# Kernel optimization log

Hardware: AMD Instinct MI355X
Metric: run time of the kernel (lower is better)

The kernel has to match this reference:

```python
import jax, jax.numpy as jnp
import numpy as np

EPS = 1e-5

def setup_inputs() -> dict:
    key = jax.random.key(0)
    ks = jax.random.split(key, 5)
    B, C_clip, Hc, Wc = 8, 768, 24, 24
    C_rs, Hr, Wr = 256, 64, 64
    clip_feat = jax.random.normal(ks[0], (B, C_clip, Hc, Wc), dtype=jnp.float32)
    rs_feat = jax.random.normal(ks[1], (B, C_rs, Hr, Wr), dtype=jnp.float32)
    ln_gamma = jnp.ones((C_clip,), dtype=jnp.float32)
    ln_beta = jnp.zeros((C_clip,), dtype=jnp.float32)
    W = jax.random.normal(ks[2], (C_rs, C_clip), dtype=jnp.float32) * (1.0 / np.sqrt(C_clip))
    b = jax.random.normal(ks[3], (C_rs,), dtype=jnp.float32) * 0.01
    alpha = jnp.array([0.5], dtype=jnp.float32)
    return {"clip_feat": clip_feat, "rs_feat": rs_feat, "ln_gamma": ln_gamma,
            "ln_beta": ln_beta, "W": W, "b": b, "alpha": alpha}

def reference(clip_feat, rs_feat, ln_gamma, ln_beta, W, b, alpha):
    B, C_clip, Hc, Wc = clip_feat.shape
    _, C_rs, Hr, Wr = rs_feat.shape
    # tokens: [B, N_clip, C_clip]
    clip_flat = clip_feat.reshape(B, C_clip, Hc * Wc).transpose(0, 2, 1)
    mu = jnp.mean(clip_flat, axis=-1, keepdims=True)
    var = jnp.var(clip_flat, axis=-1, keepdims=True)
    clip_norm = (clip_flat - mu) * jax.lax.rsqrt(var + EPS) * ln_gamma + ln_beta
    # projection to rs_dim: [B, N_clip, C_rs]
    clip_proj = jnp.einsum('bnc,dc->bnd', clip_norm, W) + b
    # rs tokens: [B, N_rs, C_rs]
    rs_flat = rs_feat.reshape(B, C_rs, Hr * Wr).transpose(0, 2, 1)
    # attn_map: [B, N_clip, N_rs], softmax over N_clip (axis=1)
    attn = jnp.einsum('bnd,bmd->bnm', clip_proj, rs_flat)
    attn = jax.nn.softmax(attn, axis=1)
    # attended: [B, N_rs, C_rs]
    attended = jnp.einsum('bnm,bnd->bmd', attn, clip_proj)
    attended = attended.transpose(0, 2, 1).reshape(B, C_rs, Hr, Wr)
    return rs_feat + alpha * attended
```

## Files before the change

kernel.cpp:

```cpp
#include <hip/hip_runtime.h>
#include <hip/hip_bf16.h>

#define EPSF 1e-5f
#define SM_OFF 60.0f

typedef short short8 __attribute__((ext_vector_type(8)));
typedef float f32x4 __attribute__((ext_vector_type(4)));

__device__ __forceinline__ short f2bf(float x) {
    __hip_bfloat16 h = __float2bfloat16(x);
    return reinterpret_cast<short&>(h);
}
__device__ __forceinline__ float bf2f(short s) {
    __hip_bfloat16 h = reinterpret_cast<__hip_bfloat16&>(s);
    return __bfloat162float(h);
}
__device__ __forceinline__ unsigned int pk2(float lo, float hi) {
    return (unsigned int)(unsigned short)f2bf(lo)
         | ((unsigned int)(unsigned short)f2bf(hi) << 16);
}
__device__ __forceinline__ void gload_lds16(const short* g, short* lds) {
    __builtin_amdgcn_global_load_lds(
        (const __attribute__((address_space(1))) unsigned int*)g,
        (__attribute__((address_space(3))) unsigned int*)lds,
        16, 0, 0);
}

__global__ __launch_bounds__(256) void w_pack_kernel(
    const float* __restrict__ W,
    short* __restrict__ Wp_hi,
    short* __restrict__ Wp_lo)
{
    int t = blockIdx.x * 256 + threadIdx.x;
    int l15 = t & 15;
    int g   = (t >> 4) & 3;
    int kt  = (t >> 6) % 24;
    int nt  = t / 1536;
    const float* src = W + (size_t)(16 * nt + l15) * 768 + 32 * kt + 8 * g;
    short8 h8, l8;
    #pragma unroll
    for (int j = 0; j < 8; ++j) {
        float w = src[j];
        short h = f2bf(w);
        h8[j] = h;
        l8[j] = f2bf(w - bf2f(h));
    }
    *reinterpret_cast<short8*>(Wp_hi + (size_t)t * 8) = h8;
    *reinterpret_cast<short8*>(Wp_lo + (size_t)t * 8) = l8;
}

__global__ __launch_bounds__(512) void ln_proj_kernel(
    const float* __restrict__ clip,
    const float* __restrict__ gamma,
    const float* __restrict__ beta,
    const short* __restrict__ Wp_hi,
    const short* __restrict__ Wp_lo,
    const float* __restrict__ bias,
    short* __restrict__ proj,
    short* __restrict__ projT)
{
    __shared__ short xh[16][776];
    __shared__ short xl[16][776];
    __shared__ float redA[8][16];
    __shared__ float redB[8][16];
    __shared__ float muS[16], rsS[16];

    const int tid = threadIdx.x;
    const int bb = blockIdx.x >> 1;
    const int dh = blockIdx.x & 1;
    const int b  = bb / 36;
    const int n0 = (bb % 36) * 16;
    const int nl = tid & 15;
    const int cg = tid >> 4;
    const int w  = tid >> 6;
    const int l  = tid & 63;
    const int l15 = l & 15;
    const int g  = l >> 4;

    const float* base = clip + (size_t)b * 768 * 576 + n0 + nl;

    float x[24];
    float s1 = 0.f, s2 = 0.f;
    #pragma unroll
    for (int i = 0; i < 24; ++i) {
        x[i] = base[(size_t)(cg + 32 * i) * 576];
        s1 += x[i]; s2 += x[i] * x[i];
    }
    s1 += __shfl_xor(s1, 16); s2 += __shfl_xor(s2, 16);
    s1 += __shfl_xor(s1, 32); s2 += __shfl_xor(s2, 32);
    if (g == 0) { redA[w][l15] = s1; redB[w][l15] = s2; }
    __syncthreads();
    if (tid < 16) {
        float a = 0.f, q = 0.f;
        #pragma unroll
        for (int k = 0; k < 8; ++k) { a += redA[k][tid]; q += redB[k][tid]; }
        float mu = a * (1.f / 768.f);
        float var = q * (1.f / 768.f) - mu * mu;
        muS[tid] = mu; rsS[tid] = rsqrtf(var + EPSF);
    }
    __syncthreads();
    {
        float mu = muS[nl], rsg = rsS[nl];
        #pragma unroll
        for (int i = 0; i < 24; ++i) {
            int c = cg + 32 * i;
            float y = (x[i] - mu) * rsg * gamma[c] + beta[c];
            short hh = f2bf(y);
            xh[nl][c] = hh;
            xl[nl][c] = f2bf(y - bf2f(hh));
        }
    }
    __syncthreads();

    const int nt = 8 * dh + w;
    f32x4 acc = f32x4{0.f, 0.f, 0.f, 0.f};
    for (int kt = 0; kt < 24; ++kt) {
        short8 ah = *reinterpret_cast<const short8*>(&xh[l15][32 * kt + 8 * g]);
        short8 al = *reinterpret_cast<const short8*>(&xl[l15][32 * kt + 8 * g]);
        size_t off = ((size_t)((nt * 24 + kt) * 64 + l)) * 8;
        short8 bh = *reinterpret_cast<const short8*>(Wp_hi + off);
        short8 bl = *reinterpret_cast<const short8*>(Wp_lo + off);
        acc = __builtin_amdgcn_mfma_f32_16x16x32_bf16(ah, bh, acc, 0, 0, 0);
        acc = __builtin_amdgcn_mfma_f32_16x16x32_bf16(al, bh, acc, 0, 0, 0);
        acc = __builtin_amdgcn_mfma_f32_16x16x32_bf16(ah, bl, acc, 0, 0, 0);
    }

    {
        int d = 16 * nt + l15;
        float bb2 = bias[d];
        #pragma unroll
        for (int r = 0; r < 4; ++r) {
            int tok = n0 + 4 * g + r;
            short v = f2bf(acc[r] + bb2);
            proj[((size_t)b * 576 + tok) * 256 + d] = v;
            projT[((size_t)b * 256 + d) * 576 + tok] = v;
        }
    }
}

__global__ __launch_bounds__(256, 2) void attn_kernel(
    const short* __restrict__ proj,
    const short* __restrict__ projT,
    const float* __restrict__ rs,
    const float* __restrict__ alpha_p,
    float* __restrict__ out)
{
    __shared__ short Ks[2][32][256];
    __shared__ short VT[2][256][32];
    __shared__ unsigned int Pb[2][2][2][16][20];
    __shared__ float Rb[2][2][2][16];

    const int tid = threadIdx.x;
    const int b  = blockIdx.x >> 6;
    const int q0 = (blockIdx.x & 63) << 6;
    const int w   = tid >> 6;
    const int l   = tid & 63;
    const int l15 = l & 15;
    const int g   = l >> 4;
    const int qh  = w >> 1;
    const int kh  = w & 1;
    const int qb  = q0 + 32 * qh;

    const short* kbase  = proj  + (size_t)b * 576 * 256;
    const short* ktbase = projT + (size_t)b * 256 * 576;
    const float* rbase  = rs + (size_t)b * 256 * 4096;
    float* obase = out + (size_t)b * 256 * 4096;

    short8 qf[2][8];
    #pragma unroll
    for (int qt = 0; qt < 2; ++qt) {
        int qg = qb + 16 * qt + l15;
        #pragma unroll
        for (int dc = 0; dc < 8; ++dc) {
            short8 v;
            #pragma unroll
            for (int j = 0; j < 8; ++j)
                v[j] = f2bf(rbase[(size_t)(32 * dc + 8 * g + j) * 4096 + qg]);
            qf[qt][dc] = v;
        }
    }

    f32x4 acc[2][8];
    #pragma unroll
    for (int qt = 0; qt < 2; ++qt)
        #pragma unroll
        for (int dt = 0; dt < 8; ++dt) acc[qt][dt] = f32x4{0.f, 0.f, 0.f, 0.f};
    float rsum[2] = {0.f, 0.f};

    auto STAGE = [&](int c, int buf) {
        #pragma unroll
        for (int i = 0; i < 4; ++i) {
            int rr = 8 * w + 2 * i + (l >> 5);
            const short* src = kbase + ((size_t)(32 * c + rr) << 8)
                             + ((((l & 31) ^ (rr & 7))) << 3);
            gload_lds16(src, &Ks[buf][8 * w + 2 * i][0]);
        }
        #pragma unroll
        for (int i = 0; i < 4; ++i) {
            int d = 64 * w + 16 * i + (l >> 2);
            const short* src = ktbase + (size_t)d * 576 + 32 * c + 8 * (l & 3);
            gload_lds16(src, &VT[buf][64 * w + 16 * i][0]);
        }
    };

    STAGE(0, 0);
    __syncthreads();

    for (int c = 0; c < 18; ++c) {
        const int cur = c & 1;

        f32x4 s0{0.f,0.f,0.f,0.f}, s1{0.f,0.f,0.f,0.f};
        __builtin_amdgcn_s_setprio(1);
        #pragma unroll
        for (int dc = 0; dc < 8; ++dc) {
            int sw = (((4 * dc + g) ^ (l15 & 7))) * 8;
            short8 kf = *reinterpret_cast<const short8*>(&Ks[cur][16 * kh + l15][sw]);
            s0 = __builtin_amdgcn_mfma_f32_16x16x32_bf16(kf, qf[0][dc], s0, 0, 0, 0);
            s1 = __builtin_amdgcn_mfma_f32_16x16x32_bf16(kf, qf[1][dc], s1, 0, 0, 0);
        }
        __builtin_amdgcn_s_setprio(0);

        float p0[4], p1[4];
        #pragma unroll
        for (int r = 0; r < 4; ++r) {
            p0[r] = __expf(s0[r] - SM_OFF);
            p1[r] = __expf(s1[r] - SM_OFF);
            rsum[0] += p0[r]; rsum[1] += p1[r];
        }
        *reinterpret_cast<uint2*>(&Pb[cur][qh][0][l15][8 * kh + 2 * g]) =
            uint2{pk2(p0[0], p0[1]), pk2(p0[2], p0[3])};
        *reinterpret_cast<uint2*>(&Pb[cur][qh][1][l15][8 * kh + 2 * g]) =
            uint2{pk2(p1[0], p1[1]), pk2(p1[2], p1[3])};

        __syncthreads();

        if (c < 17) STAGE(c + 1, cur ^ 1);

        short8 pf0 = *reinterpret_cast<const short8*>(&Pb[cur][qh][0][l15][4 * g]);
        short8 pf1 = *reinterpret_cast<const short8*>(&Pb[cur][qh][1][l15][4 * g]);
        __builtin_amdgcn_s_setprio(1);
        #pragma unroll
        for (int dt = 0; dt < 8; ++dt) {
            short8 vf = *reinterpret_cast<const short8*>(
                &VT[cur][128 * kh + 16 * dt + l15][8 * g]);
            acc[0][dt] = __builtin_amdgcn_mfma_f32_16x16x32_bf16(vf, pf0, acc[0][dt], 0, 0, 0);
            acc[1][dt] = __builtin_amdgcn_mfma_f32_16x16x32_bf16(vf, pf1, acc[1][dt], 0, 0, 0);
        }
        __builtin_amdgcn_s_setprio(0);

        if (c < 17) __syncthreads();
    }

    #pragma unroll
    for (int qt = 0; qt < 2; ++qt) {
        rsum[qt] += __shfl_xor(rsum[qt], 16);
        rsum[qt] += __shfl_xor(rsum[qt], 32);
    }
    if (g == 0) {
        Rb[qh][kh][0][l15] = rsum[0];
        Rb[qh][kh][1][l15] = rsum[1];
    }
    __syncthreads();
    float av = alpha_p[0];
    float inv0 = av / (Rb[qh][0][0][l15] + Rb[qh][1][0][l15]);
    float inv1 = av / (Rb[qh][0][1][l15] + Rb[qh][1][1][l15]);

    #pragma unroll
    for (int qt = 0; qt < 2; ++qt) {
        float inv = qt ? inv1 : inv0;
        int qg = qb + 16 * qt + l15;
        #pragma unroll
        for (int dt = 0; dt < 8; ++dt) {
            #pragma unroll
            for (int r = 0; r < 4; ++r) {
                int d = 128 * kh + 16 * dt + 4 * g + r;
                size_t idx = (size_t)d * 4096 + qg;
                obase[idx] = rbase[idx] + acc[qt][dt][r] * inv;
            }
        }
    }
}

extern "C" void kernel_launch(void* const* d_in, const int* in_sizes, int n_in,
                              void* d_out, int out_size, void* d_ws, size_t ws_size,
                              hipStream_t stream)
{
    const float* clip  = (const float*)d_in[0];
    const float* rsf   = (const float*)d_in[1];
    const float* gamma = (const float*)d_in[2];
    const float* beta  = (const float*)d_in[3];
    const float* W     = (const float*)d_in[4];
    const float* bias  = (const float*)d_in[5];
    const float* alpha = (const float*)d_in[6];
    float* out = (float*)d_out;

    char* ws = (char*)d_ws;
    short* Wp_hi = (short*)ws;
    short* Wp_lo = (short*)(ws + 393216);
    short* proj  = (short*)(ws + 786432);
    short* projT = (short*)(ws + 3145728);

    hipLaunchKernelGGL(w_pack_kernel, dim3(96), dim3(256), 0, stream, W, Wp_hi, Wp_lo);
    hipLaunchKernelGGL(ln_proj_kernel, dim3(576), dim3(512), 0, stream,
                       clip, gamma, beta, Wp_hi, Wp_lo, bias, proj, projT);
    hipLaunchKernelGGL(attn_kernel, dim3(512), dim3(256), 0, stream,
                       proj, projT, rsf, alpha, out);
}
```

Measured before the change: 72.33 us.

## Triple-buffer K/V staging with prefetch distance two and 512-thread blocks

The attention kernel moves to 512-thread blocks covering 128 queries, so each K/V chunk staged in LDS serves twice as many queries. K/V staging becomes a three-buffer ring that prefetches two chunks ahead, with each thread issuing half as many loads per stage. Full __syncthreads calls are replaced by targeted s_waitcnt vmcnt/lgkmcnt plus raw s_barrier, and the P buffer drops its double buffering. The aim is to hide global-load latency and cut redundant K/V traffic. The cost is halving the grid to 256 blocks and more LDS per block, which may reduce latency hiding across blocks.

```diff
diff --git a/kernel.cpp b/kernel.cpp
--- a/kernel.cpp
+++ b/kernel.cpp
@@ -138,21 +138,21 @@
     }
 }
 
-__global__ __launch_bounds__(256, 2) void attn_kernel(
+__global__ __launch_bounds__(512, 2) void attn_kernel(
     const short* __restrict__ proj,
     const short* __restrict__ projT,
     const float* __restrict__ rs,
     const float* __restrict__ alpha_p,
     float* __restrict__ out)
 {
-    __shared__ short Ks[2][32][256];
-    __shared__ short VT[2][256][32];
-    __shared__ unsigned int Pb[2][2][2][16][20];
-    __shared__ float Rb[2][2][2][16];
+    __shared__ short Ks[3][32][256];
+    __shared__ short VT[3][256][32];
+    __shared__ unsigned int Pb[4][2][16][20];
+    __shared__ float Rb[4][2][2][16];
 
     const int tid = threadIdx.x;
-    const int b  = blockIdx.x >> 6;
-    const int q0 = (blockIdx.x & 63) << 6;
+    const int b  = blockIdx.x >> 5;
+    const int q0 = (blockIdx.x & 31) << 7;
     const int w   = tid >> 6;
     const int l   = tid & 63;
     const int l15 = l & 15;
@@ -166,6 +166,26 @@
     const float* rbase  = rs + (size_t)b * 256 * 4096;
     float* obase = out + (size_t)b * 256 * 4096;
 
+    auto STAGE = [&](int c, int buf) {
+        #pragma unroll
+        for (int i = 0; i < 2; ++i) {
+            int row0 = 4 * w + 2 * i;
+            int rr = row0 + (l >> 5);
+            const short* src = kbase + ((size_t)(32 * c + rr) << 8)
+                             + ((((l & 31) ^ (rr & 7))) << 3);
+            gload_lds16(src, &Ks[buf][row0][0]);
+        }
+        #pragma unroll
+        for (int i = 0; i < 2; ++i) {
+            int d0 = 32 * w + 16 * i;
+            int d = d0 + (l >> 2);
+            const short* src = ktbase + (size_t)d * 576 + 32 * c + 8 * (l & 3);
+            gload_lds16(src, &VT[buf][d0][0]);
+        }
+    };
+
+    STAGE(0, 0);
+
     short8 qf[2][8];
     #pragma unroll
     for (int qt = 0; qt < 2; ++qt) {
@@ -187,28 +207,13 @@
         for (int dt = 0; dt < 8; ++dt) acc[qt][dt] = f32x4{0.f, 0.f, 0.f, 0.f};
     float rsum[2] = {0.f, 0.f};
 
-    auto STAGE = [&](int c, int buf) {
-        #pragma unroll
-        for (int i = 0; i < 4; ++i) {
-            int rr = 8 * w + 2 * i + (l >> 5);
-            const short* src = kbase + ((size_t)(32 * c + rr) << 8)
-                             + ((((l & 31) ^ (rr & 7))) << 3);
-            gload_lds16(src, &Ks[buf][8 * w + 2 * i][0]);
-        }
-        #pragma unroll
-        for (int i = 0; i < 4; ++i) {
-            int d = 64 * w + 16 * i + (l >> 2);
-            const short* src = ktbase + (size_t)d * 576 + 32 * c + 8 * (l & 3);
-            gload_lds16(src, &VT[buf][64 * w + 16 * i][0]);
-        }
-    };
-
-    STAGE(0, 0);
-    __syncthreads();
-
+    STAGE(1, 1);
+    asm volatile("s_waitcnt vmcnt(4)" ::: "memory");
+    __builtin_amdgcn_sched_barrier(0);
+    __builtin_amdgcn_s_barrier();
+
+    int cur = 0;
     for (int c = 0; c < 18; ++c) {
-        const int cur = c & 1;
-
         f32x4 s0{0.f,0.f,0.f,0.f}, s1{0.f,0.f,0.f,0.f};
         __builtin_amdgcn_s_setprio(1);
         #pragma unroll
@@ -227,17 +232,23 @@
             p1[r] = __expf(s1[r] - SM_OFF);
             rsum[0] += p0[r]; rsum[1] += p1[r];
         }
-        *reinterpret_cast<uint2*>(&Pb[cur][qh][0][l15][8 * kh + 2 * g]) =
+        *reinterpret_cast<uint2*>(&Pb[qh][0][l15][8 * kh + 2 * g]) =
             uint2{pk2(p0[0], p0[1]), pk2(p0[2], p0[3])};
-        *reinterpret_cast<uint2*>(&Pb[cur][qh][1][l15][8 * kh + 2 * g]) =
+        *reinterpret_cast<uint2*>(&Pb[qh][1][l15][8 * kh + 2 * g]) =
             uint2{pk2(p1[0], p1[1]), pk2(p1[2], p1[3])};
 
-        __syncthreads();
-
-        if (c < 17) STAGE(c + 1, cur ^ 1);
-
-        short8 pf0 = *reinterpret_cast<const short8*>(&Pb[cur][qh][0][l15][4 * g]);
-        short8 pf1 = *reinterpret_cast<const short8*>(&Pb[cur][qh][1][l15][4 * g]);
+        asm volatile("s_waitcnt lgkmcnt(0)" ::: "memory");
+        __builtin_amdgcn_sched_barrier(0);
+        __builtin_amdgcn_s_barrier();
+        __builtin_amdgcn_sched_barrier(0);
+
+        if (c < 16) {
+            int nb = cur + 2; if (nb >= 3) nb -= 3;
+            STAGE(c + 2, nb);
+        }
+
+        short8 pf0 = *reinterpret_cast<const short8*>(&Pb[qh][0][l15][4 * g]);
+        short8 pf1 = *reinterpret_cast<const short8*>(&Pb[qh][1][l15][4 * g]);
         __builtin_amdgcn_s_setprio(1);
         #pragma unroll
         for (int dt = 0; dt < 8; ++dt) {
@@ -248,7 +259,14 @@
         }
         __builtin_amdgcn_s_setprio(0);
 
-        if (c < 17) __syncthreads();
+        if (c < 17) {
+            if (c < 16) asm volatile("s_waitcnt vmcnt(4)" ::: "memory");
+            else        asm volatile("s_waitcnt vmcnt(0)" ::: "memory");
+            __builtin_amdgcn_sched_barrier(0);
+            __builtin_amdgcn_s_barrier();
+            __builtin_amdgcn_sched_barrier(0);
+        }
+        ++cur; if (cur >= 3) cur = 0;
     }
 
     #pragma unroll
@@ -303,6 +321,6 @@
     hipLaunchKernelGGL(w_pack_kernel, dim3(96), dim3(256), 0, stream, W, Wp_hi, Wp_lo);
     hipLaunchKernelGGL(ln_proj_kernel, dim3(576), dim3(512), 0, stream,
                        clip, gamma, beta, Wp_hi, Wp_lo, bias, proj, projT);
-    hipLaunchKernelGGL(attn_kernel, dim3(512), dim3(256), 0, stream,
+    hipLaunchKernelGGL(attn_kernel, dim3(256), dim3(512), 0, stream,
                        proj, projT, rsf, alpha, out);
 }
```

Measured after the change: 75.10 us. 1.04x slower.
